# Optimization experiments

Measured on AMD Instinct MI355X. Metric: run time of the kernel, lower is better.

## Reference

```python
import jax, jax.numpy as jnp
import numpy as np

MIN_NORM = 1e-15
EPS = 4e-3  # fp32 boundary epsilon used by HGCN PoincareBall


def _norm(x):
    return jnp.maximum(jnp.linalg.norm(x, axis=-1, keepdims=True), MIN_NORM)


def _artanh(x):
    return jnp.arctanh(jnp.clip(x, -1.0 + 1e-7, 1.0 - 1e-7))


def proj(x, c):
    # clip points to the open Poincare ball of curvature c
    norm = _norm(x)
    maxnorm = (1.0 - EPS) / jnp.sqrt(c)
    return jnp.where(norm > maxnorm, x / norm * maxnorm, x)


def expmap0(u, c):
    sc = jnp.sqrt(c)
    un = _norm(u)
    return jnp.tanh(sc * un) * u / (sc * un)


def logmap0(p, c):
    sc = jnp.sqrt(c)
    pn = _norm(p)
    return _artanh(sc * pn) * p / (pn * sc)


def mobius_add(x, y, c):
    x2 = jnp.sum(x * x, axis=-1, keepdims=True)
    y2 = jnp.sum(y * y, axis=-1, keepdims=True)
    xy = jnp.sum(x * y, axis=-1, keepdims=True)
    num = (1.0 + 2.0 * c * xy + c * y2) * x + (1.0 - c * x2) * y
    den = 1.0 + 2.0 * c * xy + (c ** 2) * x2 * y2
    return num / jnp.maximum(den, MIN_NORM)


def _mobius_from_mx(mx, x, c):
    # shared tail of mobius_matvec: mx is the Euclidean product, x the input points
    sc = jnp.sqrt(c)
    x_norm = _norm(x)            # [..., 1]
    mx_norm = _norm(mx)          # [..., 1]
    res = jnp.tanh(mx_norm / x_norm * _artanh(sc * x_norm)) * mx / (mx_norm * sc)
    zero_row = jnp.all(mx == 0, axis=-1, keepdims=True)
    return jnp.where(zero_row, jnp.zeros_like(res), res)


def mobius_matvec(m, x, c):
    # standard form: mx = x @ m^T   (m: [out, in], x: [N, in])
    return _mobius_from_mx(x @ m.T, x, c)


def hyp_linear(x, W, b, c):
    hw = proj(expmap0(W, c), c)             # proj_tan0 is identity on PoincareBall
    res = proj(mobius_matvec(hw, x, c), c)
    hb = proj(expmap0(b[None, :], c), c)
    return proj(mobius_add(res, hb, c), c)


def hyp_agg(h, adj, W, b, c):
    hw = proj(expmap0(W, c), c)
    support = mobius_matvec(hw, h, c)       # [N, O]
    # mobius_matvec(support, adj, c): Euclidean part is adj @ support,
    # hyperbolic rescale uses row norms of adj (the 'x' argument)
    out = _mobius_from_mx(adj @ support, adj, c)
    out = mobius_add(out, b[None, :], c)    # raw Euclidean bias, as in source
    return proj(out, c)


def hyp_act(h, c):
    xt = jax.nn.leaky_relu(logmap0(h, c))   # default slope 0.01 == F.leaky_relu
    return proj(expmap0(xt, c), 1.0 - c)    # NOTE: source projects with 1-c


def setup_inputs() -> dict:
    key = jax.random.key(0)
    kx, ka, kw1, kw2, kb2 = jax.random.split(key, 5)
    N, IN, OUT = 8192, 512, 128
    x = jax.random.normal(kx, (N, IN), dtype=jnp.float32) * 0.1
    adj = jax.random.uniform(ka, (N, N), dtype=jnp.float32) * (1.0 / N)
    c = jnp.full((1,), 0.7, dtype=jnp.float32)
    glorot = np.sqrt(6.0 / (IN + OUT))
    lin_weight = jax.random.uniform(kw1, (OUT, IN), minval=-glorot, maxval=glorot, dtype=jnp.float32)
    lin_bias = jnp.zeros((OUT,), dtype=jnp.float32)
    stdv = 1.0 / np.sqrt(OUT)
    agg_weight = jax.random.uniform(kw2, (OUT, OUT), minval=-stdv, maxval=stdv, dtype=jnp.float32)
    agg_bias = jax.random.uniform(kb2, (OUT,), minval=-stdv, maxval=stdv, dtype=jnp.float32)
    return {"x": x, "adj": adj, "c": c, "lin_weight": lin_weight, "lin_bias": lin_bias,
            "agg_weight": agg_weight, "agg_bias": agg_bias}


def reference(x, adj, c, lin_weight, lin_bias, agg_weight, agg_bias):
    h = hyp_linear(x, lin_weight, lin_bias, c)
    h = hyp_agg(h, adj, agg_weight, agg_bias, c)
    return hyp_act(h, c)
```

## Files before the change

kernel.cpp:

```cpp
#include <hip/hip_runtime.h>
#include <math.h>


#define MINN 1e-15f

typedef __bf16 bf16x8 __attribute__((ext_vector_type(8)));
typedef float  f32x4  __attribute__((ext_vector_type(4)));

__device__ __forceinline__ unsigned short f2bf(float f) {
  unsigned int u = __float_as_uint(f);
  u += 0x7FFFu + ((u >> 16) & 1u);
  return (unsigned short)(u >> 16);
}

__device__ __forceinline__ unsigned pk_trunc(float lo, float hi) {
  return __builtin_amdgcn_perm(__float_as_uint(hi), __float_as_uint(lo),
                               0x07060302u);
}

__device__ __forceinline__ float artanh_clip(float z) {
  const float B = (float)(1.0 - 1e-7);
  z = fminf(fmaxf(z, -B), B);
  return 0.5f * logf((1.0f + z) / (1.0f - z));
}

__device__ __forceinline__ float red16(float v) {
  v += __shfl_xor(v, 1, 16);
  v += __shfl_xor(v, 2, 16);
  v += __shfl_xor(v, 4, 16);
  v += __shfl_xor(v, 8, 16);
  return v;
}
__device__ __forceinline__ int red16_and(int v) {
  v &= __shfl_xor(v, 1, 16);
  v &= __shfl_xor(v, 2, 16);
  v &= __shfl_xor(v, 4, 16);
  v &= __shfl_xor(v, 8, 16);
  return v;
}

__device__ __forceinline__ float block_reduce_128(float v, float* red, int t) {
  #pragma unroll
  for (int m = 1; m < 64; m <<= 1) v += __shfl_xor(v, m, 64);
  if ((t & 63) == 0) red[t >> 6] = v;
  __syncthreads();
  return red[0] + red[1];
}

__device__ __forceinline__ size_t bswz(int k, int n) {
  return ((size_t)(((k >> 5) * 8 + (n >> 4)) * 64 + ((k >> 3) & 3) * 16 +
                   (n & 15))) * 8 + (k & 7);
}

__global__ __launch_bounds__(128) void prep_kernel(
    const float* __restrict__ lw, const float* __restrict__ aw,
    const float* __restrict__ lb, const float* __restrict__ cp,
    unsigned short* __restrict__ B1, unsigned short* __restrict__ B2,
    float* __restrict__ hb)
{
  const float c  = cp[0];
  const float sc = sqrtf(c);
  const float maxn = 0.996f / sc;
  const int b = blockIdx.x, t = threadIdx.x;
  __shared__ float red[2];

  if (b < 128) {
    const int o = b;
    float4 v = ((const float4*)(lw + (size_t)o * 512))[t];
    float ss = block_reduce_128(v.x*v.x + v.y*v.y + v.z*v.z + v.w*v.w, red, t);
    float un = fmaxf(sqrtf(ss), MINN);
    float f  = tanhf(sc * un) / (sc * un);
    float nn = f * un;
    if (nn > maxn) f *= maxn / nn;
    float vals[4] = {v.x, v.y, v.z, v.w};
    #pragma unroll
    for (int i = 0; i < 4; ++i)
      B1[bswz(4 * t + i, o)] = f2bf(f * vals[i]);
  } else if (b < 256) {
    const int n = b - 128;
    float v = aw[(size_t)n * 128 + t];
    float ss = block_reduce_128(v * v, red, t);
    float un = fmaxf(sqrtf(ss), MINN);
    float f  = tanhf(sc * un) / (sc * un);
    float nn = f * un;
    if (nn > maxn) f *= maxn / nn;
    B2[bswz(t, n)] = f2bf(f * v);
  } else {
    float v = lb[t];
    float ss = block_reduce_128(v * v, red, t);
    float un = fmaxf(sqrtf(ss), MINN);
    float f  = tanhf(sc * un) / (sc * un);
    float nn = f * un;
    if (nn > maxn) f *= maxn / nn;
    hb[t] = f * v;
  }
}

__global__ __launch_bounds__(256, 2) void hyp_fused12(
    const float* __restrict__ x, const bf16x8* __restrict__ B1f,
    const bf16x8* __restrict__ B2f, const float* __restrict__ cp,
    const float* __restrict__ hbv, unsigned short* __restrict__ B3)
{
  __shared__ __align__(16) float part[4][16][132];
  __shared__ float asw[4][16];
  __shared__ __align__(16) unsigned short h_lds[16][136];
  const int t = threadIdx.x;
  const int w = t >> 6, lane = t & 63;
  const int quad = lane >> 4, l15 = lane & 15;
  const int row0 = blockIdx.x * 16;
  const float c = cp[0], sc = sqrtf(c), maxn = 0.996f / sc;

  f32x4 acc[8] = {};
  float as4[4] = {};
  const float*  Ap = x + (size_t)(row0 + l15) * 512 + w * 128 + quad * 8;
  const bf16x8* Bp = B1f + (size_t)(w * 4) * 512 + lane;

  #pragma unroll
  for (int s = 0; s < 4; ++s) {
    float4 x0 = *(const float4*)(Ap + s * 32);
    float4 x1 = *(const float4*)(Ap + s * 32 + 4);
    as4[0] = fmaf(x0.x, x0.x, fmaf(x0.y, x0.y, as4[0]));
    as4[1] = fmaf(x0.z, x0.z, fmaf(x0.w, x0.w, as4[1]));
    as4[2] = fmaf(x1.x, x1.x, fmaf(x1.y, x1.y, as4[2]));
    as4[3] = fmaf(x1.z, x1.z, fmaf(x1.w, x1.w, as4[3]));
    union { unsigned short us[8]; bf16x8 v; } pk;
    pk.us[0] = f2bf(x0.x); pk.us[1] = f2bf(x0.y);
    pk.us[2] = f2bf(x0.z); pk.us[3] = f2bf(x0.w);
    pk.us[4] = f2bf(x1.x); pk.us[5] = f2bf(x1.y);
    pk.us[6] = f2bf(x1.z); pk.us[7] = f2bf(x1.w);
    #pragma unroll
    for (int i = 0; i < 8; ++i)
      acc[i] = __builtin_amdgcn_mfma_f32_16x16x32_bf16(
                   pk.v, Bp[(size_t)s * 512 + i * 64], acc[i], 0, 0, 0);
  }
  float asum = (as4[0] + as4[1]) + (as4[2] + as4[3]);
  asum += __shfl_xor(asum, 16, 64);
  asum += __shfl_xor(asum, 32, 64);
  #pragma unroll
  for (int i = 0; i < 8; ++i)
    #pragma unroll
    for (int r = 0; r < 4; ++r)
      part[w][quad * 4 + r][i * 16 + l15] = acc[i][r];
  if (lane < 16) asw[w][l15] = asum;
  __syncthreads();

  const int row = t >> 4, j0 = t & 15;
  float v[8];
  #pragma unroll
  for (int i = 0; i < 8; ++i)
    v[i] = part[0][row][j0 * 8 + i] + part[1][row][j0 * 8 + i]
         + part[2][row][j0 * 8 + i] + part[3][row][j0 * 8 + i];
  const float xss = asw[0][row] + asw[1][row] + asw[2][row] + asw[3][row];

  float mxss_l = 0.f; int zf = 1;
  #pragma unroll
  for (int i = 0; i < 8; ++i) { mxss_l += v[i] * v[i]; zf &= (v[i] == 0.f); }
  const float mxss = red16(mxss_l);
  zf = red16_and(zf);

  const float xn  = fmaxf(sqrtf(xss), MINN);
  const float mxn = fmaxf(sqrtf(mxss), MINN);
  float f1 = 0.f;
  if (!zf) f1 = tanhf(mxn / xn * artanh_clip(sc * xn)) / (mxn * sc);

  float g = f1;
  {
    float rn = f1 * mxn;
    if (rn > maxn) g = f1 * (maxn / rn);
  }
  float yv[8];
  {
    float4 q0 = ((const float4*)hbv)[j0 * 2];
    float4 q1 = ((const float4*)hbv)[j0 * 2 + 1];
    yv[0]=q0.x; yv[1]=q0.y; yv[2]=q0.z; yv[3]=q0.w;
    yv[4]=q1.x; yv[5]=q1.y; yv[6]=q1.z; yv[7]=q1.w;
  }
  float xy_l = 0.f, y2_l = 0.f, o8[8];
  #pragma unroll
  for (int i = 0; i < 8; ++i) {
    o8[i] = g * v[i];
    xy_l += o8[i] * yv[i];
    y2_l += yv[i] * yv[i];
  }
  const float xy = red16(xy_l), y2 = red16(y2_l);
  const float x2 = g * g * mxss;
  const float den = fmaxf(1.0f + 2.0f * c * xy + c * c * x2 * y2, MINN);
  const float ca = (1.0f + 2.0f * c * xy + c * y2) / den;
  const float cb = (1.0f - c * x2) / den;
  float h8[8]; float hss_l = 0.f;
  #pragma unroll
  for (int i = 0; i < 8; ++i) {
    h8[i] = ca * o8[i] + cb * yv[i];
    hss_l += h8[i] * h8[i];
  }
  const float hss = red16(hss_l);
  const float hn  = fmaxf(sqrtf(hss), MINN);
  const float s2  = (hn > maxn) ? maxn / hn : 1.0f;
  const float hn2 = fmaxf(s2 * hn, MINN);

  {
    union { unsigned short us[8]; uint4 q; } hp;
    #pragma unroll
    for (int i = 0; i < 8; ++i) hp.us[i] = f2bf(s2 * h8[i]);
    *(uint4*)&h_lds[row][j0 * 8] = hp.q;
  }
  __syncthreads();

  const bf16x8 av2 = *(const bf16x8*)&h_lds[l15][w * 32 + quad * 8];
  f32x4 acc2[8] = {};
  #pragma unroll
  for (int i = 0; i < 8; ++i)
    acc2[i] = __builtin_amdgcn_mfma_f32_16x16x32_bf16(
                  av2, B2f[(size_t)(w * 8 + i) * 64 + lane], acc2[i], 0, 0, 0);
  #pragma unroll
  for (int i = 0; i < 8; ++i)
    #pragma unroll
    for (int r = 0; r < 4; ++r)
      part[w][quad * 4 + r][i * 16 + l15] = acc2[i][r];
  __syncthreads();

  float v2[8];
  #pragma unroll
  for (int i = 0; i < 8; ++i)
    v2[i] = part[0][row][j0 * 8 + i] + part[1][row][j0 * 8 + i]
          + part[2][row][j0 * 8 + i] + part[3][row][j0 * 8 + i];
  float m2l = 0.f; int zf2 = 1;
  #pragma unroll
  for (int i = 0; i < 8; ++i) { m2l += v2[i] * v2[i]; zf2 &= (v2[i] == 0.f); }
  const float mx2ss = red16(m2l);
  zf2 = red16_and(zf2);
  const float mx2n = fmaxf(sqrtf(mx2ss), MINN);
  float f2 = 0.f;
  if (!zf2) f2 = tanhf(mx2n / hn2 * artanh_clip(sc * hn2)) / (mx2n * sc);

  const int k = row0 + row;
  const size_t base = ((size_t)(((k >> 5) * 8 + (j0 >> 1)) * 64 +
                       ((k >> 3) & 3) * 16 + 8 * (j0 & 1))) * 8 + (k & 7);
  #pragma unroll
  for (int i = 0; i < 8; ++i)
    B3[base + (size_t)i * 8] = f2bf(f2 * v2[i]);
}

__global__ __launch_bounds__(512, 2) void hyp_gemm3(
    const float* __restrict__ A, const bf16x8* __restrict__ Bf,
    const float* __restrict__ cp, const float* __restrict__ yvec,
    float* __restrict__ out)
{
  __shared__ __align__(16) unsigned short a_lds[2][32][264];
  const int t = threadIdx.x;
  const int w = t >> 6, lane = t & 63;
  const int quad = lane >> 4, l15 = lane & 15;
  const int row0 = blockIdx.x * 32;
  const float c = cp[0], sc = sqrtf(c), maxn = 0.996f / sc;

  f32x4 acc[2] = {};
  float as4[4] = {};
  const float*  Ap = A + (size_t)(row0 + 4 * w) * 8192 + lane * 4;
  const bf16x8* Bw = Bf + (size_t)w * 64 + lane;

  {
    float4 aR[4];
    #pragma unroll
    for (int j = 0; j < 4; ++j) aR[j] = *(const float4*)(Ap + j * 8192);
    #pragma unroll
    for (int j = 0; j < 4; ++j) {
      as4[j] = fmaf(aR[j].x, aR[j].x, fmaf(aR[j].y, aR[j].y,
               fmaf(aR[j].z, aR[j].z, fmaf(aR[j].w, aR[j].w, as4[j]))));
      *(uint2*)&a_lds[0][4 * w + j][lane * 4] =
          make_uint2(pk_trunc(aR[j].x, aR[j].y), pk_trunc(aR[j].z, aR[j].w));
    }
  }
  __syncthreads();

  for (int win = 0; win < 32; ++win) {
    const int cur = win & 1;
    bf16x8 b[8];
    #pragma unroll
    for (int ks = 0; ks < 8; ++ks)
      b[ks] = Bw[(size_t)(win * 8 + ks) * 512];
    float4 aR[4];
    if (win < 31) {
      #pragma unroll
      for (int j = 0; j < 4; ++j)
        aR[j] = *(const float4*)(Ap + j * 8192 + (size_t)(win + 1) * 256);
    }
    #pragma unroll
    for (int ks = 0; ks < 8; ++ks) {
      bf16x8 af0 = *(const bf16x8*)&a_lds[cur][l15][ks * 32 + quad * 8];
      bf16x8 af1 = *(const bf16x8*)&a_lds[cur][l15 + 16][ks * 32 + quad * 8];
      acc[0] = __builtin_amdgcn_mfma_f32_16x16x32_bf16(af0, b[ks], acc[0],
                                                       0, 0, 0);
      acc[1] = __builtin_amdgcn_mfma_f32_16x16x32_bf16(af1, b[ks], acc[1],
                                                       0, 0, 0);
    }
    if (win < 31) {
      #pragma unroll
      for (int j = 0; j < 4; ++j) {
        as4[j] = fmaf(aR[j].x, aR[j].x, fmaf(aR[j].y, aR[j].y,
                 fmaf(aR[j].z, aR[j].z, fmaf(aR[j].w, aR[j].w, as4[j]))));
        *(uint2*)&a_lds[cur ^ 1][4 * w + j][lane * 4] =
            make_uint2(pk_trunc(aR[j].x, aR[j].y), pk_trunc(aR[j].z, aR[j].w));
      }
    }
    __syncthreads();
  }

  float (*part)[132] = (float (*)[132]) & a_lds[0][0][0];
  float* asw = (float*)&a_lds[0][0][0] + 32 * 132;

  #pragma unroll
  for (int i = 0; i < 2; ++i)
    #pragma unroll
    for (int r = 0; r < 4; ++r)
      part[16 * i + quad * 4 + r][16 * w + l15] = acc[i][r];
  #pragma unroll
  for (int j = 0; j < 4; ++j) {
    float s = as4[j];
    #pragma unroll
    for (int m = 1; m < 64; m <<= 1) s += __shfl_xor(s, m, 64);
    if (lane == 0) asw[4 * w + j] = s;
  }
  __syncthreads();

  const int row = t >> 4, j0 = t & 15;
  float v[8];
  {
    float4 q0 = *(const float4*)&part[row][j0 * 8];
    float4 q1 = *(const float4*)&part[row][j0 * 8 + 4];
    v[0]=q0.x; v[1]=q0.y; v[2]=q0.z; v[3]=q0.w;
    v[4]=q1.x; v[5]=q1.y; v[6]=q1.z; v[7]=q1.w;
  }
  const float xss = asw[row];

  float mxss_l = 0.f; int zf = 1;
  #pragma unroll
  for (int i = 0; i < 8; ++i) { mxss_l += v[i] * v[i]; zf &= (v[i] == 0.f); }
  const float mxss = red16(mxss_l);
  zf = red16_and(zf);

  const float xn  = fmaxf(sqrtf(xss), MINN);
  const float mxn = fmaxf(sqrtf(mxss), MINN);
  float f1 = 0.f;
  if (!zf) f1 = tanhf(mxn / xn * artanh_clip(sc * xn)) / (mxn * sc);

  float yv[8];
  {
    float4 q0 = ((const float4*)yvec)[j0 * 2];
    float4 q1 = ((const float4*)yvec)[j0 * 2 + 1];
    yv[0]=q0.x; yv[1]=q0.y; yv[2]=q0.z; yv[3]=q0.w;
    yv[4]=q1.x; yv[5]=q1.y; yv[6]=q1.z; yv[7]=q1.w;
  }

  float xy_l = 0.f, y2_l = 0.f, o8[8];
  #pragma unroll
  for (int i = 0; i < 8; ++i) {
    o8[i] = f1 * v[i];
    xy_l += o8[i] * yv[i];
    y2_l += yv[i] * yv[i];
  }
  const float xy = red16(xy_l), y2 = red16(y2_l);
  const float x2 = f1 * f1 * mxss;
  const float den = fmaxf(1.0f + 2.0f * c * xy + c * c * x2 * y2, MINN);
  const float ca = (1.0f + 2.0f * c * xy + c * y2) / den;
  const float cb = (1.0f - c * x2) / den;
  float h8[8]; float hss_l = 0.f;
  #pragma unroll
  for (int i = 0; i < 8; ++i) {
    h8[i] = ca * o8[i] + cb * yv[i];
    hss_l += h8[i] * h8[i];
  }
  const float hss = red16(hss_l);
  const float hn  = fmaxf(sqrtf(hss), MINN);
  const float s2  = (hn > maxn) ? maxn / hn : 1.0f;

  const float pn = fmaxf(s2 * hn, MINN);
  const float lf = artanh_clip(sc * pn) / (pn * sc);
  float xt[8]; float uss_l = 0.f;
  #pragma unroll
  for (int i = 0; i < 8; ++i) {
    float l = lf * (s2 * h8[i]);
    xt[i] = (l >= 0.f) ? l : 0.01f * l;
    uss_l += xt[i] * xt[i];
  }
  const float uss = red16(uss_l);
  const float un  = fmaxf(sqrtf(uss), MINN);
  const float ef  = tanhf(sc * un) / (sc * un);
  const float on  = ef * un;
  const float maxn2 = 0.996f / sqrtf(1.0f - c);
  const float s3 = (on > maxn2) ? maxn2 / on : 1.0f;

  float* orow = out + (size_t)(row0 + row) * 128 + j0 * 8;
  *(float4*)orow =
      make_float4(s3*ef*xt[0], s3*ef*xt[1], s3*ef*xt[2], s3*ef*xt[3]);
  *(float4*)(orow + 4) =
      make_float4(s3*ef*xt[4], s3*ef*xt[5], s3*ef*xt[6], s3*ef*xt[7]);
}

extern "C" void kernel_launch(void* const* d_in, const int* in_sizes, int n_in,
                              void* d_out, int out_size, void* d_ws, size_t ws_size,
                              hipStream_t stream)
{
  const float* x   = (const float*)d_in[0];
  const float* adj = (const float*)d_in[1];
  const float* cp  = (const float*)d_in[2];
  const float* lw  = (const float*)d_in[3];
  const float* lb  = (const float*)d_in[4];
  const float* aw  = (const float*)d_in[5];
  const float* ab  = (const float*)d_in[6];
  float* out = (float*)d_out;

  char* ws = (char*)d_ws;
  unsigned short* B1sw = (unsigned short*)(ws);
  unsigned short* B2sw = (unsigned short*)(ws + 131072);
  unsigned short* B3sw = (unsigned short*)(ws + 163840);
  float*          hb   = (float*)(ws + 2260992);

  prep_kernel<<<257, 128, 0, stream>>>(lw, aw, lb, cp, B1sw, B2sw, hb);
  hyp_fused12<<<512, 256, 0, stream>>>(x, (const bf16x8*)B1sw,
                                       (const bf16x8*)B2sw, cp, hb, B3sw);
  hyp_gemm3<<<256, 512, 0, stream>>>(adj, (const bf16x8*)B3sw, cp, ab, out);
}
```

Baseline: 404.1 us.

## Prefetch adj tiles two windows ahead and use lighter LDS-only barriers

The adj-streaming GEMM now holds the next window's fp32 A values in registers (aP) and issues global loads two windows ahead, writing the converted bf16 tile to LDS before the MFMA loop rather than after it. The per-window __syncthreads is replaced by an explicit lgkmcnt wait plus s_barrier, so the barrier no longer waits for outstanding global (vmcnt) loads. This is meant to hide HBM latency of the 8192x8192 adj stream behind the MFMA work, at the cost of extra VGPRs under the 512x2 launch bounds.

```diff
diff --git a/kernel.cpp b/kernel.cpp
--- a/kernel.cpp
+++ b/kernel.cpp
@@ -258,19 +258,25 @@
   const float*  Ap = A + (size_t)(row0 + 4 * w) * 8192 + lane * 4;
   const bf16x8* Bw = Bf + (size_t)w * 64 + lane;
 
-  {
-    float4 aR[4];
-    #pragma unroll
-    for (int j = 0; j < 4; ++j) aR[j] = *(const float4*)(Ap + j * 8192);
+  float4 aP[4];
+  {
+    float4 aT[4];
+    #pragma unroll
+    for (int j = 0; j < 4; ++j) aT[j] = *(const float4*)(Ap + j * 8192);
+    #pragma unroll
+    for (int j = 0; j < 4; ++j)
+      aP[j] = *(const float4*)(Ap + j * 8192 + 256);
     #pragma unroll
     for (int j = 0; j < 4; ++j) {
-      as4[j] = fmaf(aR[j].x, aR[j].x, fmaf(aR[j].y, aR[j].y,
-               fmaf(aR[j].z, aR[j].z, fmaf(aR[j].w, aR[j].w, as4[j]))));
+      as4[j] = fmaf(aT[j].x, aT[j].x, fmaf(aT[j].y, aT[j].y,
+               fmaf(aT[j].z, aT[j].z, fmaf(aT[j].w, aT[j].w, as4[j]))));
       *(uint2*)&a_lds[0][4 * w + j][lane * 4] =
-          make_uint2(pk_trunc(aR[j].x, aR[j].y), pk_trunc(aR[j].z, aR[j].w));
+          make_uint2(pk_trunc(aT[j].x, aT[j].y), pk_trunc(aT[j].z, aT[j].w));
     }
   }
-  __syncthreads();
+  asm volatile("s_waitcnt lgkmcnt(0)" ::: "memory");
+  __builtin_amdgcn_s_barrier();
+  asm volatile("" ::: "memory");
 
   for (int win = 0; win < 32; ++win) {
     const int cur = win & 1;
@@ -278,11 +284,20 @@
     #pragma unroll
     for (int ks = 0; ks < 8; ++ks)
       b[ks] = Bw[(size_t)(win * 8 + ks) * 512];
-    float4 aR[4];
     if (win < 31) {
       #pragma unroll
-      for (int j = 0; j < 4; ++j)
-        aR[j] = *(const float4*)(Ap + j * 8192 + (size_t)(win + 1) * 256);
+      for (int j = 0; j < 4; ++j) {
+        as4[j] = fmaf(aP[j].x, aP[j].x, fmaf(aP[j].y, aP[j].y,
+                 fmaf(aP[j].z, aP[j].z, fmaf(aP[j].w, aP[j].w, as4[j]))));
+        *(uint2*)&a_lds[cur ^ 1][4 * w + j][lane * 4] =
+            make_uint2(pk_trunc(aP[j].x, aP[j].y),
+                       pk_trunc(aP[j].z, aP[j].w));
+      }
+      if (win < 30) {
+        #pragma unroll
+        for (int j = 0; j < 4; ++j)
+          aP[j] = *(const float4*)(Ap + j * 8192 + (size_t)(win + 2) * 256);
+      }
     }
     #pragma unroll
     for (int ks = 0; ks < 8; ++ks) {
@@ -293,16 +308,9 @@
       acc[1] = __builtin_amdgcn_mfma_f32_16x16x32_bf16(af1, b[ks], acc[1],
                                                        0, 0, 0);
     }
-    if (win < 31) {
-      #pragma unroll
-      for (int j = 0; j < 4; ++j) {
-        as4[j] = fmaf(aR[j].x, aR[j].x, fmaf(aR[j].y, aR[j].y,
-                 fmaf(aR[j].z, aR[j].z, fmaf(aR[j].w, aR[j].w, as4[j]))));
-        *(uint2*)&a_lds[cur ^ 1][4 * w + j][lane * 4] =
-            make_uint2(pk_trunc(aR[j].x, aR[j].y), pk_trunc(aR[j].z, aR[j].w));
-      }
-    }
-    __syncthreads();
+    asm volatile("s_waitcnt lgkmcnt(0)" ::: "memory");
+    __builtin_amdgcn_s_barrier();
+    asm volatile("" ::: "memory");
   }
 
   float (*part)[132] = (float (*)[132]) & a_lds[0][0][0];
```

Result: no change. 401.9 us (-0.5%).
